# Optimization experiments

Measured on AMD Instinct MI355X. Metric: run time of the kernel, lower is better.

Reference implementation:

```python
import jax, jax.numpy as jnp
import numpy as np

N_NODES = 50000
N_EDGES = 625000
D = 128


def setup_inputs() -> dict:
    key = jax.random.key(0)
    kx, ks, kr, kw, kb = jax.random.split(key, 5)
    x = jax.random.normal(kx, (N_NODES, D), dtype=jnp.float32)
    senders = jax.random.randint(ks, (N_EDGES,), 0, N_NODES, dtype=jnp.int64)
    receivers = jax.random.randint(kr, (N_EDGES,), 0, N_NODES, dtype=jnp.int64)
    # nn.Linear(2*D, D): weight [D, 2*D], bias [D]
    lim = 1.0 / np.sqrt(2 * D)
    W = jax.random.uniform(kw, (D, 2 * D), minval=-lim, maxval=lim, dtype=jnp.float32)
    b = jax.random.uniform(kb, (D,), minval=-lim, maxval=lim, dtype=jnp.float32)
    return {"x": x, "senders": senders, "receivers": receivers, "n_nodes": N_NODES, "W": W, "b": b}


def reference(x, senders, receivers, n_nodes, W, b):
    # Add self loops (with_self=True)
    self_idx = jnp.arange(n_nodes, dtype=senders.dtype)
    s = jnp.concatenate([senders, self_idx])   # [E + N]
    r = jnp.concatenate([receivers, self_idx]) # [E + N]

    ones = jnp.ones(r.shape[0], dtype=x.dtype)
    # degree_norm=True branch (note: mirrors the original's naming exactly:
    # 'out_degree' counted over receivers, 'in_degree' over senders)
    out_degree = jax.ops.segment_sum(ones, r, num_segments=n_nodes)  # [N]
    in_degree = jax.ops.segment_sum(ones, s, num_segments=n_nodes)   # [N]
    out_degree_norm = jax.lax.rsqrt(jnp.maximum(out_degree, 1.0))
    in_degree_norm = jax.lax.rsqrt(jnp.maximum(in_degree, 1.0))

    # Gather sender embeddings, scale, scatter-add to receivers
    sender_emb = x[s] * out_degree_norm[s][:, None]  # [E+N, D]
    aggregated = jax.ops.segment_sum(sender_emb, r, num_segments=n_nodes)  # [N, D]

    # edge_count over receivers == out_degree (same scatter), clamped
    edge_count = jnp.maximum(out_degree, 1.0)
    aggregated = aggregated / edge_count[:, None]
    aggregated = aggregated * in_degree_norm[:, None]

    combined = jnp.concatenate([x, aggregated], axis=1)  # [N, 2D]
    return combined @ W.T + b
```

## Files before the change

kernel.cpp:

```cpp
#include <hip/hip_runtime.h>

#define DIM 128
#define BM 128
#define BK 32
#define BINSZ 128
#define EPB 2048
#define AGS 136

typedef __attribute__((ext_vector_type(8))) short short8;
typedef __attribute__((ext_vector_type(4))) float f32x4;

__device__ __forceinline__ unsigned short f2bf(float f) {
    unsigned int b = __float_as_uint(f);
    return (unsigned short)((b + 0x7fffu + ((b >> 16) & 1u)) >> 16);
}
__device__ __forceinline__ float bf_lo(unsigned int u) { return __uint_as_float(u << 16); }
__device__ __forceinline__ float bf_hi(unsigned int u) { return __uint_as_float(u & 0xffff0000u); }
__device__ __forceinline__ unsigned int pack2(float a, float b) {
    return (unsigned int)f2bf(a) | ((unsigned int)f2bf(b) << 16);
}
__device__ __forceinline__ uint2 pack4(float4 v) {
    uint2 r; r.x = pack2(v.x, v.y); r.y = pack2(v.z, v.w); return r;
}

__global__ __launch_bounds__(256) void convert_hist_kernel(
        const float4* __restrict__ x4, const float4* __restrict__ W4,
        const int* __restrict__ senders, const int* __restrict__ receivers,
        uint2* __restrict__ xb4, uint2* __restrict__ Wb4,
        int* __restrict__ Hr, int* __restrict__ Hs, int* __restrict__ done,
        int nx4, int nw4, int E, int nbin, int NAB) {
    if ((int)blockIdx.x < NAB) {
        __shared__ int hr[512], hs[512];
        int t = threadIdx.x;
        if (blockIdx.x == 0 && t == 0) *done = 0;
        for (int b = t; b < nbin; b += 256) { hr[b] = 0; hs[b] = 0; }
        __syncthreads();
        int base = blockIdx.x * EPB;
        for (int k = 0; k < EPB; k += 256) {
            int e = base + k + t;
            if (e < E) {
                atomicAdd(&hr[receivers[e] >> 7], 1);
                atomicAdd(&hs[senders[e] >> 7], 1);
            }
        }
        __syncthreads();
        size_t ho = (size_t)blockIdx.x * nbin;
        for (int b = t; b < nbin; b += 256) { Hr[ho + b] = hr[b]; Hs[ho + b] = hs[b]; }
    } else {
        int i = ((int)blockIdx.x - NAB) * 256 + threadIdx.x;
        if (i < nx4) xb4[i] = pack4(x4[i]);
        if (i < nw4) Wb4[i] = pack4(W4[i]);
    }
}

__global__ __launch_bounds__(512) void scan_kernel(
        int* __restrict__ Hr, int* __restrict__ Hs,
        int* __restrict__ tot_r, int* __restrict__ tot_s,
        int* __restrict__ base_r, int* __restrict__ base_s,
        int* __restrict__ row_start, int* __restrict__ done,
        int NAB, int nbin, int N, int E) {
    __shared__ int sr[512], ss[512];
    __shared__ int rank_sh;
    int b = blockIdx.x, t = threadIdx.x;
    int vr = (t < NAB) ? Hr[(size_t)t * nbin + b] : 0;
    int vs = (t < NAB) ? Hs[(size_t)t * nbin + b] : 0;
    sr[t] = vr; ss[t] = vs;
    __syncthreads();
    for (int off = 1; off < 512; off <<= 1) {
        int ur = (t >= off) ? sr[t - off] : 0;
        int us = (t >= off) ? ss[t - off] : 0;
        __syncthreads();
        sr[t] += ur; ss[t] += us;
        __syncthreads();
    }
    if (t < NAB) {
        Hr[(size_t)t * nbin + b] = sr[t] - vr;
        Hs[(size_t)t * nbin + b] = ss[t] - vs;
    }
    if (t == 511) {
        tot_r[b] = sr[511]; tot_s[b] = ss[511];
        __threadfence();
        rank_sh = atomicAdd(done, 1);
    }
    __syncthreads();
    if (rank_sh == (int)gridDim.x - 1) {
        int wr2 = (t < nbin) ? atomicAdd(&tot_r[t], 0) : 0;
        int ws2 = (t < nbin) ? atomicAdd(&tot_s[t], 0) : 0;
        sr[t] = wr2; ss[t] = ws2;
        __syncthreads();
        for (int off = 1; off < 512; off <<= 1) {
            int ur = (t >= off) ? sr[t - off] : 0;
            int us = (t >= off) ? ss[t - off] : 0;
            __syncthreads();
            sr[t] += ur; ss[t] += us;
            __syncthreads();
        }
        if (t < nbin) { base_r[t] = sr[t] - wr2; base_s[t] = ss[t] - ws2; }
        if (t == 0) { base_r[nbin] = E; base_s[nbin] = E; row_start[N] = E; }
    }
}

__global__ __launch_bounds__(256) void scatter_kernel(
        const int* __restrict__ senders, const int* __restrict__ receivers,
        const int* __restrict__ Hr, const int* __restrict__ Hs,
        const int* __restrict__ base_r, const int* __restrict__ base_s,
        unsigned int* __restrict__ bucket_r, unsigned short* __restrict__ bucket_s,
        int E, int nbin) {
    __shared__ int br_[512], bs_[512];
    int t = threadIdx.x;
    size_t ho = (size_t)blockIdx.x * nbin;
    for (int b = t; b < nbin; b += 256) {
        br_[b] = base_r[b] + Hr[ho + b];
        bs_[b] = base_s[b] + Hs[ho + b];
    }
    __syncthreads();
    int base = blockIdx.x * EPB;
    for (int k = 0; k < EPB; k += 256) {
        int e = base + k + t;
        if (e < E) {
            int s = senders[e], r = receivers[e];
            int pr = atomicAdd(&br_[r >> 7], 1);
            bucket_r[pr] = ((unsigned int)(r & 127) << 16) | (unsigned int)s;
            int ps = atomicAdd(&bs_[s >> 7], 1);
            bucket_s[ps] = (unsigned short)s;
        }
    }
}

__global__ __launch_bounds__(256) void fine_kernel(
        const unsigned int* __restrict__ bucket_r,
        const unsigned short* __restrict__ bucket_s,
        const int* __restrict__ base_r,
        const int* __restrict__ base_s,
        const uint2* __restrict__ xb2,
        int* __restrict__ edge_src,
        int* __restrict__ row_start,
        float* __restrict__ fs,
        uint2* __restrict__ xs2,
        int N) {
    __shared__ int fine[BINSZ], fstart[BINSZ], cs[BINSZ];
    __shared__ float scs[BINSZ];
    int b = blockIdx.x, t = threadIdx.x;
    if (t < BINSZ) { fine[t] = 0; cs[t] = 0; }
    __syncthreads();

    int loR = base_r[b], hiR = base_r[b + 1];
    int loS = base_s[b], hiS = base_s[b + 1];
    for (int i = loR + t; i < hiR; i += 256)
        atomicAdd(&fine[bucket_r[i] >> 16], 1);
    for (int i = loS + t; i < hiS; i += 256)
        atomicAdd(&cs[bucket_s[i] & 127], 1);
    __syncthreads();

    if (t < BINSZ) fstart[t] = fine[t];
    __syncthreads();
    for (int off = 1; off < BINSZ; off <<= 1) {
        int u = (t < BINSZ && t >= off) ? fstart[t - off] : 0;
        __syncthreads();
        if (t < BINSZ) fstart[t] += u;
        __syncthreads();
    }
    if (t < BINSZ) {
        int excl = fstart[t] - fine[t];
        int node = b * BINSZ + t;
        float od = (float)(fine[t] + 1);
        float sc = rsqrtf(od);
        scs[t] = sc;
        if (node < N) {
            row_start[node] = loR + excl;
            fs[node] = rsqrtf((float)(cs[t] + 1)) / od;
        }
        fstart[t] = excl;
    }
    __syncthreads();

    for (int i = loR + t; i < hiR; i += 256) {
        unsigned int u = bucket_r[i];
        int pos = atomicAdd(&fstart[u >> 16], 1);
        edge_src[loR + pos] = (int)(u & 0xFFFFu);
    }

    int nrow0 = b * BINSZ;
    for (int idx = t; idx < BINSZ * 32; idx += 256) {
        int row = idx >> 5, c = idx & 31;
        int node = nrow0 + row;
        if (node < N) {
            float sc = scs[row];
            uint2 u = xb2[(size_t)node * 32 + c];
            uint2 o;
            o.x = pack2(bf_lo(u.x) * sc, bf_hi(u.x) * sc);
            o.y = pack2(bf_lo(u.y) * sc, bf_hi(u.y) * sc);
            xs2[(size_t)node * 32 + c] = o;
        }
    }
}

__global__ __launch_bounds__(512) void gather_gemm_kernel(
        const unsigned short* __restrict__ x_bf,
        const unsigned int* __restrict__ xs,
        const int* __restrict__ edge_src,
        const int* __restrict__ row_start,
        const float* __restrict__ fs,
        const unsigned short* __restrict__ W_bf,
        const float* __restrict__ bias,
        float* __restrict__ out, int N) {
    __shared__ unsigned short Agg[BM * AGS];
    __shared__ unsigned short As[BM * BK];
    __shared__ unsigned short Bs[DIM * BK];

    int t = threadIdx.x, lane = t & 63, w = t >> 6;
    int row0 = blockIdx.x * BM;

    for (int i = 0; i < 16; i++) {
        int row = w * 16 + i;
        int n = row0 + row;
        float ax = 0.f, ay = 0.f;
        if (n < N) {
            int start = row_start[n];
            int deg   = row_start[n + 1] - start;
            for (int base = 0; base < deg; base += 64) {
                int cnt = deg - base; if (cnt > 64) cnt = 64;
                int src = 0;
                if (lane < cnt) src = edge_src[start + base + lane];
                int j = 0;
                for (; j + 8 <= cnt; j += 8) {
                    int ssx[8]; unsigned int uu[8];
#pragma unroll
                    for (int q = 0; q < 8; q++) ssx[q] = __shfl(src, j + q);
#pragma unroll
                    for (int q = 0; q < 8; q++) uu[q] = xs[(size_t)ssx[q] * 64 + lane];
#pragma unroll
                    for (int q = 0; q < 8; q++) { ax += bf_lo(uu[q]); ay += bf_hi(uu[q]); }
                }
                for (; j < cnt; j++) {
                    int s = __shfl(src, j);
                    unsigned int u = xs[(size_t)s * 64 + lane];
                    ax += bf_lo(u); ay += bf_hi(u);
                }
            }
            float f = fs[n];
            unsigned int u = xs[(size_t)n * 64 + lane];
            ax = (ax + bf_lo(u)) * f;
            ay = (ay + bf_hi(u)) * f;
        }
        *(unsigned int*)&Agg[row * AGS + 2 * lane] = pack2(ax, ay);
    }
    __syncthreads();

    int wr = w >> 2, wc = w & 3;
    f32x4 acc[4][2];
#pragma unroll
    for (int i = 0; i < 4; i++)
#pragma unroll
        for (int j = 0; j < 2; j++) acc[i][j] = (f32x4){0.f, 0.f, 0.f, 0.f};

    for (int kt = 0; kt < 8; kt++) {
        if (kt < 4) {
            int row = t >> 2, ch = t & 3;
            uint4 v = *(const uint4*)&x_bf[(size_t)(row0 + row) * 128 + kt * BK + ch * 8];
            *(uint4*)&As[row * BK + ch * 8] = v;
        }
        {
            int n2 = t >> 2, ch = t & 3;
            uint4 v = *(const uint4*)&W_bf[(size_t)n2 * 256 + kt * BK + ch * 8];
            *(uint4*)&Bs[n2 * BK + ch * 8] = v;
        }
        __syncthreads();

        short8 a[4], b2[2];
#pragma unroll
        for (int i = 0; i < 4; i++) {
            int arow = wr * 64 + i * 16 + (lane & 15);
            a[i] = (kt < 4)
                ? *(const short8*)&As[arow * BK + (lane >> 4) * 8]
                : *(const short8*)&Agg[arow * AGS + (kt - 4) * 32 + (lane >> 4) * 8];
        }
#pragma unroll
        for (int j = 0; j < 2; j++)
            b2[j] = *(const short8*)&Bs[(wc * 32 + j * 16 + (lane & 15)) * BK + (lane >> 4) * 8];
#pragma unroll
        for (int i = 0; i < 4; i++)
#pragma unroll
            for (int j = 0; j < 2; j++)
                acc[i][j] = __builtin_amdgcn_mfma_f32_16x16x32_bf16(a[i], b2[j], acc[i][j], 0, 0, 0);
        __syncthreads();
    }

    int cq = lane >> 4;
    int cl = lane & 15;
#pragma unroll
    for (int j = 0; j < 2; j++) {
        int col = wc * 32 + j * 16 + cl;
        float bb = bias[col];
#pragma unroll
        for (int i = 0; i < 4; i++) {
            int rbase = row0 + wr * 64 + i * 16 + cq * 4;
#pragma unroll
            for (int r = 0; r < 4; r++) {
                int row = rbase + r;
                if (row < N) out[(size_t)row * DIM + col] = acc[i][j][r] + bb;
            }
        }
    }
}

extern "C" void kernel_launch(void* const* d_in, const int* in_sizes, int n_in,
                              void* d_out, int out_size, void* d_ws, size_t ws_size,
                              hipStream_t stream) {
    const float* x         = (const float*)d_in[0];
    const int*   senders   = (const int*)d_in[1];
    const int*   receivers = (const int*)d_in[2];
    const float* W         = (const float*)d_in[4];
    const float* bias      = (const float*)d_in[5];
    float*       out       = (float*)d_out;

    int N    = in_sizes[0] / DIM;
    int E    = in_sizes[1];
    int nbin = (N + BINSZ - 1) / BINSZ;
    int NAB  = (E + EPB - 1) / EPB;
    int NP   = ((N + BM - 1) / BM) * BM;

    char* ws = (char*)d_ws;
    size_t off = 0;
    #define WS_ALLOC(ptrtype, name, bytes) \
        ptrtype name = (ptrtype)(ws + off); off += (((size_t)(bytes)) + 255) & ~(size_t)255;
    WS_ALLOC(int*,            tot_r,     (size_t)nbin * 4)
    WS_ALLOC(int*,            tot_s,     (size_t)nbin * 4)
    WS_ALLOC(int*,            base_r,    (size_t)(nbin + 1) * 4)
    WS_ALLOC(int*,            base_s,    (size_t)(nbin + 1) * 4)
    WS_ALLOC(int*,            row_start, (size_t)(N + 1) * 4)
    WS_ALLOC(float*,          fs,        (size_t)N * 4)
    WS_ALLOC(int*,            done,      256)
    WS_ALLOC(int*,            edge_src,  (size_t)E * 4)
    WS_ALLOC(unsigned short*, x_bf,      (size_t)NP * DIM * 2)
    WS_ALLOC(unsigned short*, xs_bf,     (size_t)NP * DIM * 2)
    WS_ALLOC(unsigned short*, W_bf,      (size_t)DIM * 256 * 2)
    WS_ALLOC(unsigned int*,   bucket_r,  (size_t)E * 4)
    WS_ALLOC(unsigned short*, bucket_s,  (size_t)E * 2)
    WS_ALLOC(int*,            Hr,        (size_t)NAB * nbin * 4)
    WS_ALLOC(int*,            Hs,        (size_t)NAB * nbin * 4)
    #undef WS_ALLOC

    int nx4 = N * 32;
    int nw4 = DIM * 256 / 4;
    int conv_blocks = (nx4 + 255) / 256;

    convert_hist_kernel<<<NAB + conv_blocks, 256, 0, stream>>>(
        (const float4*)x, (const float4*)W, senders, receivers,
        (uint2*)x_bf, (uint2*)W_bf, Hr, Hs, done, nx4, nw4, E, nbin, NAB);
    scan_kernel<<<nbin, 512, 0, stream>>>(Hr, Hs, tot_r, tot_s, base_r, base_s,
                                          row_start, done, NAB, nbin, N, E);
    scatter_kernel<<<NAB, 256, 0, stream>>>(senders, receivers, Hr, Hs,
                                            base_r, base_s, bucket_r, bucket_s, E, nbin);
    fine_kernel<<<nbin, 256, 0, stream>>>(bucket_r, bucket_s, base_r, base_s,
                                          (const uint2*)x_bf, edge_src, row_start,
                                          fs, (uint2*)xs_bf, N);
    gather_gemm_kernel<<<(N + BM - 1) / BM, 512, 0, stream>>>(
        x_bf, (const unsigned int*)xs_bf, edge_src, row_start, fs,
        W_bf, bias, out, N);
}
```

Measured before the change: 206.3 us.

## Split fused gather-GEMM into separate gather and GEMM kernels

Moves the neighbor aggregation out of the GEMM kernel into a standalone one-wavefront-per-node gather kernel that writes bf16 aggregates to global memory, then runs a plain GEMM reading both halves from global. This removes the large LDS aggregate buffer and the serial 16-rows-per-wave gather inside the GEMM blocks, aiming for higher occupancy and better latency hiding in the gather. It adds an extra launch and a global round trip for the aggregate, and reuses the aggregate buffer as scratch for earlier bucket/histogram arrays.

```diff
diff --git a/kernel.cpp b/kernel.cpp
--- a/kernel.cpp
+++ b/kernel.cpp
@@ -5,7 +5,6 @@
 #define BK 32
 #define BINSZ 128
 #define EPB 2048
-#define AGS 136
 
 typedef __attribute__((ext_vector_type(8))) short short8;
 typedef __attribute__((ext_vector_type(4))) float f32x4;
@@ -195,59 +194,64 @@
     }
 }
 
-__global__ __launch_bounds__(512) void gather_gemm_kernel(
-        const unsigned short* __restrict__ x_bf,
+__global__ __launch_bounds__(256) void gather_kernel(
         const unsigned int* __restrict__ xs,
         const int* __restrict__ edge_src,
         const int* __restrict__ row_start,
         const float* __restrict__ fs,
+        unsigned int* __restrict__ aggb,
+        int N) {
+    int lane = threadIdx.x & 63;
+    int n = (blockIdx.x * blockDim.x + threadIdx.x) >> 6;
+    if (n >= N) return;
+
+    int start = row_start[n];
+    int deg   = row_start[n + 1] - start;
+    float ax = 0.f, ay = 0.f;
+
+    for (int base = 0; base < deg; base += 64) {
+        int cnt = deg - base; if (cnt > 64) cnt = 64;
+        int src = 0;
+        if (lane < cnt) src = edge_src[start + base + lane];
+        int j = 0;
+        for (; j + 8 <= cnt; j += 8) {
+            int ss[8]; unsigned int uu[8];
+#pragma unroll
+            for (int q = 0; q < 8; q++) ss[q] = __shfl(src, j + q);
+#pragma unroll
+            for (int q = 0; q < 8; q++) uu[q] = xs[(size_t)ss[q] * 64 + lane];
+#pragma unroll
+            for (int q = 0; q < 8; q++) { ax += bf_lo(uu[q]); ay += bf_hi(uu[q]); }
+        }
+        for (; j < cnt; j++) {
+            int s = __shfl(src, j);
+            unsigned int u = xs[(size_t)s * 64 + lane];
+            ax += bf_lo(u); ay += bf_hi(u);
+        }
+    }
+
+    float f = fs[n];
+    unsigned int u = xs[(size_t)n * 64 + lane];
+    ax = (ax + bf_lo(u)) * f;
+    ay = (ay + bf_hi(u)) * f;
+    aggb[(size_t)n * 64 + lane] = pack2(ax, ay);
+}
+
+__global__ __launch_bounds__(512) void gemm_kernel(
+        const unsigned short* __restrict__ x_bf,
+        const unsigned short* __restrict__ agg_bf,
         const unsigned short* __restrict__ W_bf,
         const float* __restrict__ bias,
         float* __restrict__ out, int N) {
-    __shared__ unsigned short Agg[BM * AGS];
     __shared__ unsigned short As[BM * BK];
     __shared__ unsigned short Bs[DIM * BK];
 
-    int t = threadIdx.x, lane = t & 63, w = t >> 6;
+    int t    = threadIdx.x;
+    int lane = t & 63;
+    int w    = t >> 6;
+    int wr   = w >> 2, wc = w & 3;
     int row0 = blockIdx.x * BM;
 
-    for (int i = 0; i < 16; i++) {
-        int row = w * 16 + i;
-        int n = row0 + row;
-        float ax = 0.f, ay = 0.f;
-        if (n < N) {
-            int start = row_start[n];
-            int deg   = row_start[n + 1] - start;
-            for (int base = 0; base < deg; base += 64) {
-                int cnt = deg - base; if (cnt > 64) cnt = 64;
-                int src = 0;
-                if (lane < cnt) src = edge_src[start + base + lane];
-                int j = 0;
-                for (; j + 8 <= cnt; j += 8) {
-                    int ssx[8]; unsigned int uu[8];
-#pragma unroll
-                    for (int q = 0; q < 8; q++) ssx[q] = __shfl(src, j + q);
-#pragma unroll
-                    for (int q = 0; q < 8; q++) uu[q] = xs[(size_t)ssx[q] * 64 + lane];
-#pragma unroll
-                    for (int q = 0; q < 8; q++) { ax += bf_lo(uu[q]); ay += bf_hi(uu[q]); }
-                }
-                for (; j < cnt; j++) {
-                    int s = __shfl(src, j);
-                    unsigned int u = xs[(size_t)s * 64 + lane];
-                    ax += bf_lo(u); ay += bf_hi(u);
-                }
-            }
-            float f = fs[n];
-            unsigned int u = xs[(size_t)n * 64 + lane];
-            ax = (ax + bf_lo(u)) * f;
-            ay = (ay + bf_hi(u)) * f;
-        }
-        *(unsigned int*)&Agg[row * AGS + 2 * lane] = pack2(ax, ay);
-    }
-    __syncthreads();
-
-    int wr = w >> 2, wc = w & 3;
     f32x4 acc[4][2];
 #pragma unroll
     for (int i = 0; i < 4; i++)
@@ -255,34 +259,32 @@
         for (int j = 0; j < 2; j++) acc[i][j] = (f32x4){0.f, 0.f, 0.f, 0.f};
 
     for (int kt = 0; kt < 8; kt++) {
-        if (kt < 4) {
+        const unsigned short* src = (kt < 4) ? x_bf : agg_bf;
+        int k0 = (kt & 3) * BK;
+        {
             int row = t >> 2, ch = t & 3;
-            uint4 v = *(const uint4*)&x_bf[(size_t)(row0 + row) * 128 + kt * BK + ch * 8];
+            uint4 v = *(const uint4*)&src[(size_t)(row0 + row) * 128 + k0 + ch * 8];
             *(uint4*)&As[row * BK + ch * 8] = v;
         }
         {
-            int n2 = t >> 2, ch = t & 3;
-            uint4 v = *(const uint4*)&W_bf[(size_t)n2 * 256 + kt * BK + ch * 8];
-            *(uint4*)&Bs[n2 * BK + ch * 8] = v;
-        }
-        __syncthreads();
-
-        short8 a[4], b2[2];
-#pragma unroll
-        for (int i = 0; i < 4; i++) {
-            int arow = wr * 64 + i * 16 + (lane & 15);
-            a[i] = (kt < 4)
-                ? *(const short8*)&As[arow * BK + (lane >> 4) * 8]
-                : *(const short8*)&Agg[arow * AGS + (kt - 4) * 32 + (lane >> 4) * 8];
-        }
+            int n = t >> 2, ch = t & 3;
+            uint4 v = *(const uint4*)&W_bf[(size_t)n * 256 + kt * BK + ch * 8];
+            *(uint4*)&Bs[n * BK + ch * 8] = v;
+        }
+        __syncthreads();
+
+        short8 a[4], b[2];
+#pragma unroll
+        for (int i = 0; i < 4; i++)
+            a[i] = *(const short8*)&As[(wr * 64 + i * 16 + (lane & 15)) * BK + (lane >> 4) * 8];
 #pragma unroll
         for (int j = 0; j < 2; j++)
-            b2[j] = *(const short8*)&Bs[(wc * 32 + j * 16 + (lane & 15)) * BK + (lane >> 4) * 8];
+            b[j] = *(const short8*)&Bs[(wc * 32 + j * 16 + (lane & 15)) * BK + (lane >> 4) * 8];
 #pragma unroll
         for (int i = 0; i < 4; i++)
 #pragma unroll
             for (int j = 0; j < 2; j++)
-                acc[i][j] = __builtin_amdgcn_mfma_f32_16x16x32_bf16(a[i], b2[j], acc[i][j], 0, 0, 0);
+                acc[i][j] = __builtin_amdgcn_mfma_f32_16x16x32_bf16(a[i], b[j], acc[i][j], 0, 0, 0);
         __syncthreads();
     }
 
@@ -334,12 +336,17 @@
     WS_ALLOC(int*,            edge_src,  (size_t)E * 4)
     WS_ALLOC(unsigned short*, x_bf,      (size_t)NP * DIM * 2)
     WS_ALLOC(unsigned short*, xs_bf,     (size_t)NP * DIM * 2)
+    WS_ALLOC(unsigned short*, agg_bf,    (size_t)NP * DIM * 2)
     WS_ALLOC(unsigned short*, W_bf,      (size_t)DIM * 256 * 2)
-    WS_ALLOC(unsigned int*,   bucket_r,  (size_t)E * 4)
-    WS_ALLOC(unsigned short*, bucket_s,  (size_t)E * 2)
-    WS_ALLOC(int*,            Hr,        (size_t)NAB * nbin * 4)
-    WS_ALLOC(int*,            Hs,        (size_t)NAB * nbin * 4)
     #undef WS_ALLOC
+
+    size_t eb = ((size_t)E * 4 + 255) & ~(size_t)255;
+    size_t sb = ((size_t)E * 2 + 255) & ~(size_t)255;
+    size_t hb = ((size_t)NAB * nbin * 4 + 255) & ~(size_t)255;
+    unsigned int*   bucket_r = (unsigned int*)agg_bf;
+    unsigned short* bucket_s = (unsigned short*)((char*)agg_bf + eb);
+    int*            Hr       = (int*)((char*)agg_bf + eb + sb);
+    int*            Hs       = (int*)((char*)agg_bf + eb + sb + hb);
 
     int nx4 = N * 32;
     int nw4 = DIM * 256 / 4;
@@ -355,7 +362,9 @@
     fine_kernel<<<nbin, 256, 0, stream>>>(bucket_r, bucket_s, base_r, base_s,
                                           (const uint2*)x_bf, edge_src, row_start,
                                           fs, (uint2*)xs_bf, N);
-    gather_gemm_kernel<<<(N + BM - 1) / BM, 512, 0, stream>>>(
-        x_bf, (const unsigned int*)xs_bf, edge_src, row_start, fs,
-        W_bf, bias, out, N);
-}
+    gather_kernel<<<(N * 64 + 255) / 256, 256, 0, stream>>>(
+        (const unsigned int*)xs_bf, edge_src, row_start, fs,
+        (unsigned int*)agg_bf, N);
+    gemm_kernel<<<(N + BM - 1) / BM, 512, 0, stream>>>(
+        x_bf, agg_bf, W_bf, bias, out, N);
+}
```

Result: faster. 186.4 us (-9.6%).
